# Kernel tuning notes

Hardware: AMD Instinct MI355X
Metric: run time of the kernel (lower is better)

Reference implementation:

```python
import jax, jax.numpy as jnp
import numpy as np

N_HEAD = 8


def build_mask(T, N):
    """Boolean mask [L, L], True = blocked. Mirrors the torch st_mask construction
    for text_mask_mode='part_only', text_to_motion_attn=False, all domains present."""
    L = 3 * T + 5 * N
    motion = 3 * T
    m = np.zeros((L, L), dtype=bool)
    # motion x motion: start fully blocked, then carve block-causal structure
    m[:motion, :motion] = True
    causal = np.tril(np.ones((T, T), dtype=bool))          # incl. diagonal
    strict = np.tril(np.ones((T, T), dtype=bool), k=-1)    # strictly lower
    m[0:T, 0:T] = ~causal
    m[T:2*T, 0:T] = ~causal
    m[T:2*T, T:2*T] = ~strict
    m[T:2*T, 2*T:3*T] = ~strict
    m[2*T:3*T, 0:T] = ~causal
    m[2*T:3*T, T:2*T] = ~causal
    m[2*T:3*T, 2*T:3*T] = ~strict
    # motion queries cannot see text keys
    m[:motion, motion:] = True
    # text queries cannot see motion keys (text_to_motion_attn=False)
    m[motion:, :motion] = True
    # part_only: upper-body rows see upper/torso/whole/simple_tag text domains;
    # lower-body rows see lower/torso/whole/simple_tag text domains
    ts = motion
    up, down = slice(T, 2*T), slice(2*T, 3*T)
    for d in (0, 2, 3, 4):
        m[up, ts + d*N: ts + (d+1)*N] = False
    for d in (1, 2, 3, 4):
        m[down, ts + d*N: ts + (d+1)*N] = False
    # text x text region stays all-False (full attention among text tokens)
    return jnp.asarray(m)


def setup_inputs() -> dict:
    key = jax.random.key(0)
    ks = jax.random.split(key, 9)
    B, T_motion, N, C = 2, 1024, 64, 512
    L = 3 * T_motion + 5 * N
    s = 1.0 / np.sqrt(C)
    return {
        "x": jax.random.normal(ks[0], (B, L, C), dtype=jnp.float32),
        "Wq": jax.random.normal(ks[1], (C, C), dtype=jnp.float32) * s,
        "bq": jnp.zeros((C,), dtype=jnp.float32),
        "Wk": jax.random.normal(ks[2], (C, C), dtype=jnp.float32) * s,
        "bk": jnp.zeros((C,), dtype=jnp.float32),
        "Wv": jax.random.normal(ks[3], (C, C), dtype=jnp.float32) * s,
        "bv": jnp.zeros((C,), dtype=jnp.float32),
        "Wp": jax.random.normal(ks[4], (C, C), dtype=jnp.float32) * s,
        "bp": jnp.zeros((C,), dtype=jnp.float32),
        "T_motion": T_motion,
        "N": N,
    }


def reference(x, Wq, bq, Wk, bk, Wv, bv, Wp, bp, T_motion, N):
    B, L, C = x.shape
    H = N_HEAD
    dh = C // H
    mask = build_mask(int(T_motion), int(N))  # [L, L] bool, True = blocked

    def split_heads(t):  # [B, L, C] -> [B, H, L, dh]
        return t.reshape(B, L, H, dh).transpose(0, 2, 1, 3)

    q = split_heads(x @ Wq + bq)
    k = split_heads(x @ Wk + bk)
    v = split_heads(x @ Wv + bv)

    att = jnp.einsum("bhqd,bhkd->bhqk", q, k) * (1.0 / np.sqrt(dh))
    att = jnp.where(mask[None, None], -jnp.inf, att)
    att = jax.nn.softmax(att, axis=-1)
    y = jnp.einsum("bhqk,bhkd->bhqd", att, v)
    y = y.transpose(0, 2, 1, 3).reshape(B, L, C)
    return y @ Wp + bp
```

## Files before the change

kernel.cpp:

```cpp
#include <hip/hip_runtime.h>
#include <hip/hip_bf16.h>
#include <math.h>

typedef __attribute__((ext_vector_type(8))) short bf16x8;
typedef __attribute__((ext_vector_type(4))) short short4v;
typedef __attribute__((ext_vector_type(4))) float f32x4;

#define DEVI __device__ __forceinline__

constexpr int Bb  = 2;
constexpr int Tm  = 1024;
constexpr int Ntx = 64;
constexpr int Hh  = 8;
constexpr int Ll  = 3*Tm + 5*Ntx;
constexpr int Mm  = Bb*Ll;
constexpr int MOT = 3*Tm;
constexpr int UPH = 75;
constexpr int PST = 72;

DEVI short f2b(float f) {
  unsigned u = __builtin_bit_cast(unsigned, f);
  u = u + 0x7fffu + ((u >> 16) & 1u);
  return (short)(u >> 16);
}

DEVI void gld16(const void* g, void* l) {
  __builtin_amdgcn_global_load_lds(
      (const __attribute__((address_space(1))) unsigned*)g,
      (__attribute__((address_space(3))) unsigned*)l, 16, 0, 0);
}

DEVI f32x4 mfma16(bf16x8 a, bf16x8 b, f32x4 c) {
  return __builtin_amdgcn_mfma_f32_16x16x32_bf16(a, b, c, 0, 0, 0);
}


__global__ __launch_bounds__(256) void cast_x_kern(const float* __restrict__ x,
                                                   short* __restrict__ xb) {
  int i = (blockIdx.x*256 + threadIdx.x)*4;
  float4 v = *(const float4*)(x + i);
  short4v r;
  r.x = f2b(v.x); r.y = f2b(v.y); r.z = f2b(v.z); r.w = f2b(v.w);
  *(short4v*)(xb + i) = r;
}

__global__ __launch_bounds__(256) void prep_w_kern(
    const float* __restrict__ Wq, const float* __restrict__ Wk,
    const float* __restrict__ Wv, const float* __restrict__ Wp,
    short* __restrict__ WtQKV, short* __restrict__ WpT) {
  int idx = blockIdx.x*256 + threadIdx.x;
  int mat = idx >> 18;
  int n = (idx >> 9) & 511;
  int k = idx & 511;
  const float* W = (mat == 0) ? Wq : (mat == 1) ? Wk : (mat == 2) ? Wv : Wp;
  short s = f2b(W[k*512 + n]);
  if (mat < 3) WtQKV[((size_t)(mat*512 + n))*512 + k] = s;
  else         WpT[(size_t)n*512 + k] = s;
}


template<int MODE>
__global__ __launch_bounds__(256) void gemm_bt(
    const short* __restrict__ A, const short* __restrict__ Bt,
    const float* __restrict__ bias_q, const float* __restrict__ bias_k,
    const float* __restrict__ bias_v,
    short* __restrict__ Qb, short* __restrict__ Kb, short* __restrict__ Vt,
    float* __restrict__ outf) {
  __shared__ __align__(16) short At[128*32];
  __shared__ __align__(16) short Bs[128*32];
  const int tid = threadIdx.x;
  const int w = tid >> 6, lane = tid & 63;
  const int col = lane & 15, g = lane >> 4;
  const int tm = blockIdx.x, tn = blockIdx.y;
  const int wm = w >> 1, wn = w & 1;

  f32x4 acc[4][4] = {};

  for (int k0 = 0; k0 < 512; k0 += 32) {
    __syncthreads();
#pragma unroll
    for (int it = 0; it < 2; ++it) {
      int e0 = w*512 + it*2048 + lane*8;
      int row = e0 >> 5, cc = e0 & 31;
      gld16(A  + (size_t)(tm*128 + row)*512 + k0 + cc, At + w*512 + it*2048);
      gld16(Bt + (size_t)(tn*128 + row)*512 + k0 + cc, Bs + w*512 + it*2048);
    }
    __syncthreads();
    bf16x8 af[4], bfr[4];
#pragma unroll
    for (int i = 0; i < 4; ++i)
      af[i] = *(const bf16x8*)(At + (wm*64 + i*16 + col)*32 + g*8);
#pragma unroll
    for (int j = 0; j < 4; ++j)
      bfr[j] = *(const bf16x8*)(Bs + (wn*64 + j*16 + col)*32 + g*8);
#pragma unroll
    for (int i = 0; i < 4; ++i)
#pragma unroll
      for (int j = 0; j < 4; ++j)
        acc[i][j] = mfma16(af[i], bfr[j], acc[i][j]);
  }

#pragma unroll
  for (int i = 0; i < 4; ++i) {
    int mbase = tm*128 + wm*64 + i*16 + g*4;
#pragma unroll
    for (int j = 0; j < 4; ++j) {
      int ncol = tn*128 + wn*64 + j*16 + col;
#pragma unroll
      for (int r = 0; r < 4; ++r) {
        int mrow = mbase + r;
        float v = acc[i][j][r];
        if constexpr (MODE == 0) {
          float bias = (ncol < 512) ? bias_q[ncol]
                     : (ncol < 1024) ? bias_k[ncol - 512] : bias_v[ncol - 1024];
          v += bias;
          int bb = (mrow >= Ll) ? 1 : 0;
          int lpos = mrow - bb*Ll;
          int nn = ncol & 511;
          int h = nn >> 6, dd = nn & 63;
          int bh = bb*8 + h;
          short s = f2b(v);
          if (ncol < 512)        Qb[((size_t)(bh*Ll + lpos))*64 + dd] = s;
          else if (ncol < 1024)  Kb[((size_t)(bh*Ll + lpos))*64 + dd] = s;
          else                   Vt[((size_t)(bh*64 + dd))*Ll + lpos] = s;
        } else {
          outf[(size_t)mrow*512 + ncol] = v + bias_q[ncol];
        }
      }
    }
  }
}


__global__ __launch_bounds__(256) void attn_kern(
    const short* __restrict__ Qb, const short* __restrict__ Kb,
    const short* __restrict__ Vt, float* __restrict__ slots,
    short* __restrict__ attout) {
  __shared__ __align__(16) short Kls[2][4096];
  __shared__ __align__(16) short Vls[2][4096];
  __shared__ __align__(16) short Pls[4][32*PST];
  const int tid = threadIdx.x;
  const int w = tid >> 6, lane = tid & 63;
  const int col = lane & 15, g = lane >> 4;

  const int v  = (blockIdx.x & 7)*150 + (blockIdx.x >> 3);
  const int bh = v / UPH;
  const int lr = v - bh*UPH;

  int qsec, seg = 0, j = 0, t3 = 0;
  if (lr < 56) {
    int jj = lr/7, s = lr - jj*7;
    j = 7 - jj;
    if (s == 0)      qsec = 0;
    else if (s <= 3) { qsec = 1; seg = s - 1; }
    else             { qsec = 2; seg = s - 4; }
  } else if (lr < 72) {
    int t = lr - 56; qsec = 1 + (t & 1); j = t >> 1; seg = 3;
  } else { qsec = 3; t3 = lr - 72; }

  const int q0b = (qsec < 3) ? qsec*Tm + j*128 : MOT + ((t3 == 2) ? 192 : t3*128);
  const int t0w = j*128 + w*32;
  const int q0w = q0b + w*32;

  int kbase = 0, off = 0, nb;
  bool masked;
  if (qsec == 3)      { kbase = MOT;  nb = 5;       masked = false; }
  else if (qsec == 0) { kbase = 0;    nb = 2*j + 2; masked = true; off = 0; }
  else if (seg == 0)  { kbase = 0;    nb = 2*j + 2; masked = true; off = 0; }
  else if (seg == 1)  { kbase = Tm;   nb = 2*j + 2; masked = true; off = (qsec == 1) ? 1 : 0; }
  else if (seg == 2)  { kbase = 2*Tm; nb = 2*j + 2; masked = true; off = 1; }
  else                { kbase = 0;    nb = 4;       masked = false; }

  auto keyof = [&](int i) -> int {
    if (qsec == 3) return MOT + i*64;
    if (!masked) { int d = (i == 0) ? ((qsec == 1) ? 0 : 1) : i + 1; return MOT + d*64; }
    return kbase + i*64;
  };

  const short* Kbase_ = Kb + (size_t)bh*Ll*64;
  const short* Vbase_ = Vt + (size_t)bh*64*Ll;

  bf16x8 aq[2][2];
#pragma unroll
  for (int qf = 0; qf < 2; ++qf) {
    const short* p = Qb + ((size_t)bh*Ll + q0w + qf*16 + col)*64;
    aq[qf][0] = *(const bf16x8*)(p + g*8);
    aq[qf][1] = *(const bf16x8*)(p + 32 + g*8);
  }

  float ls[2][4] = {};
  f32x4 out[2][4] = {};
  constexpr float SCl = 0.125f * 1.44269504f;

  auto stage = [&](int buf, int key0) {
#pragma unroll
    for (int it = 0; it < 2; ++it) {
      int L = it*4096 + tid*16;
      int row = L >> 7;
      int sw = (row & 7) << 4;
      gld16((const char*)Kbase_ + (size_t)key0*128 + (L ^ sw),
            (char*)&Kls[buf][0] + it*4096 + w*1024);
      gld16((const char*)(Vbase_ + (size_t)row*Ll + key0) + ((L & 127) ^ sw),
            (char*)&Vls[buf][0] + it*4096 + w*1024);
    }
  };

  auto compute = [&](int buf, int i) {
    const int swc = (col & 7) << 4;
    f32x4 s[2][4];
#pragma unroll
    for (int kk = 0; kk < 4; ++kk) {
      const char* base = (const char*)&Kls[buf][0] + (kk*16 + col)*128;
      bf16x8 k0 = *(const bf16x8*)(base + ((g*16) ^ swc));
      bf16x8 k1 = *(const bf16x8*)(base + ((64 + g*16) ^ swc));
#pragma unroll
      for (int qf = 0; qf < 2; ++qf) {
        f32x4 t = {0,0,0,0};
        t = mfma16(aq[qf][0], k0, t);
        t = mfma16(aq[qf][1], k1, t);
        s[qf][kk] = t;
      }
    }
    const bool dm = masked && (i*64 + 63 + off > t0w);
    short* pw = &Pls[w][0];
#pragma unroll
    for (int qf = 0; qf < 2; ++qf)
#pragma unroll
      for (int kk = 0; kk < 4; ++kk)
#pragma unroll
        for (int r = 0; r < 4; ++r) {
          float p = __builtin_amdgcn_exp2f(s[qf][kk][r]*SCl);
          if (dm && (i*64 + kk*16 + col + off > t0w + qf*16 + g*4 + r)) p = 0.f;
          ls[qf][r] += p;
          pw[(qf*16 + g*4 + r)*PST + kk*16 + col] = f2b(p);
        }
    bf16x8 pa[2][2];
#pragma unroll
    for (int qf = 0; qf < 2; ++qf) {
      const short* base = &Pls[w][0] + (qf*16 + col)*PST;
      pa[qf][0] = *(const bf16x8*)(base + g*8);
      pa[qf][1] = *(const bf16x8*)(base + 32 + g*8);
    }
#pragma unroll
    for (int ch = 0; ch < 4; ++ch) {
      const char* base = (const char*)&Vls[buf][0] + (ch*16 + col)*128;
      bf16x8 v0 = *(const bf16x8*)(base + ((g*16) ^ swc));
      bf16x8 v1 = *(const bf16x8*)(base + ((64 + g*16) ^ swc));
#pragma unroll
      for (int qf = 0; qf < 2; ++qf) {
        out[qf][ch] = mfma16(pa[qf][0], v0, out[qf][ch]);
        out[qf][ch] = mfma16(pa[qf][1], v1, out[qf][ch]);
      }
    }
  };

  stage(0, keyof(0));
  for (int i = 0; i < nb; ++i) {
    if (i + 1 < nb) {
      stage((i + 1) & 1, keyof(i + 1));
      asm volatile("s_waitcnt vmcnt(4)" ::: "memory");
    } else {
      asm volatile("s_waitcnt vmcnt(0)" ::: "memory");
    }
    __builtin_amdgcn_sched_barrier(0);
    __builtin_amdgcn_s_barrier();
    bool skip = masked && (t0w + 31 < i*64 + off);
    if (!skip) compute(i & 1, i);
    __builtin_amdgcn_s_barrier();
  }

  float rs[2][4];
#pragma unroll
  for (int qf = 0; qf < 2; ++qf)
#pragma unroll
    for (int r = 0; r < 4; ++r) {
      float t = ls[qf][r];
      t += __shfl_xor(t, 1); t += __shfl_xor(t, 2);
      t += __shfl_xor(t, 4); t += __shfl_xor(t, 8);
      rs[qf][r] = t;
    }

  if (qsec == 1 || qsec == 2) {
    float* sp = slots + ((((size_t)bh*2 + (qsec - 1))*8 + j)*4 + seg)*8320;
#pragma unroll
    for (int qf = 0; qf < 2; ++qf) {
#pragma unroll
      for (int ch = 0; ch < 4; ++ch)
#pragma unroll
        for (int r = 0; r < 4; ++r)
          sp[(w*32 + qf*16 + g*4 + r)*64 + ch*16 + col] = out[qf][ch][r];
      if (col == 0)
#pragma unroll
        for (int r = 0; r < 4; ++r)
          sp[8192 + w*32 + qf*16 + g*4 + r] = rs[qf][r];
    }
  } else {
    const int b = bh >> 3, h = bh & 7;
#pragma unroll
    for (int qf = 0; qf < 2; ++qf)
#pragma unroll
      for (int r = 0; r < 4; ++r) {
        float inv = 1.0f / rs[qf][r];
        size_t rowoff = ((size_t)(b*Ll + q0w + qf*16 + g*4 + r))*512 + h*64;
#pragma unroll
        for (int ch = 0; ch < 4; ++ch)
          attout[rowoff + ch*16 + col] = f2b(out[qf][ch][r]*inv);
      }
  }
}

__global__ __launch_bounds__(256) void fin_kern(const float* __restrict__ slots,
                                                short* __restrict__ attout) {
  const int w = threadIdx.x >> 6, lane = threadIdx.x & 63;
  const int ridx = blockIdx.x*4 + w;
  const int bh = ridx >> 11;
  const int rr = ridx & 2047;
  const int qsec = 1 + (rr >> 10);
  const int rl = rr & 1023;
  const int j = rl >> 7;
  const int row_local = rl & 127;
  const float* base = slots + (((size_t)bh*2 + (qsec - 1))*8 + j)*4*8320;
  float a = 0.f, l = 0.f;
#pragma unroll
  for (int s = 0; s < 4; ++s) {
    a += base[s*8320 + row_local*64 + lane];
    l += base[s*8320 + 8192 + row_local];
  }
  const int b = bh >> 3, h = bh & 7;
  attout[((size_t)(b*Ll + qsec*Tm + rl))*512 + h*64 + lane] = f2b(a / l);
}


extern "C" void kernel_launch(void* const* d_in, const int* in_sizes, int n_in,
                              void* d_out, int out_size, void* d_ws, size_t ws_size,
                              hipStream_t stream) {
  const float* x  = (const float*)d_in[0];
  const float* Wq = (const float*)d_in[1];
  const float* bq = (const float*)d_in[2];
  const float* Wk = (const float*)d_in[3];
  const float* bk = (const float*)d_in[4];
  const float* Wv = (const float*)d_in[5];
  const float* bv = (const float*)d_in[6];
  const float* Wp = (const float*)d_in[7];
  const float* bp = (const float*)d_in[8];
  float* out = (float*)d_out;

  short* ws = (short*)d_ws;
  constexpr size_t SZ  = (size_t)Mm*512;
  short* xb    = ws;
  short* WtQKV = xb + SZ;
  short* WpT   = WtQKV + (size_t)1536*512;
  short* Qb    = WpT + (size_t)512*512;
  short* Kb    = Qb + SZ;
  short* Vt    = Kb + SZ;
  short* att   = Vt + SZ;
  float* slots = (float*)(att + SZ);

  cast_x_kern<<<dim3(Mm*512/1024), dim3(256), 0, stream>>>(x, xb);
  prep_w_kern<<<dim3(4096), dim3(256), 0, stream>>>(Wq, Wk, Wv, Wp, WtQKV, WpT);
  gemm_bt<0><<<dim3(53, 12), dim3(256), 0, stream>>>(xb, WtQKV, bq, bk, bv,
                                                     Qb, Kb, Vt, nullptr);
  attn_kern<<<dim3(1200), dim3(256), 0, stream>>>(Qb, Kb, Vt, slots, att);
  fin_kern<<<dim3(8192), dim3(256), 0, stream>>>(slots, att);
  gemm_bt<1><<<dim3(53, 4), dim3(256), 0, stream>>>(att, WpT, bp, nullptr, nullptr,
                                                    nullptr, nullptr, nullptr, out);
}
```

Before: 109.5 us.

## Fold softmax scale into Q and transpose score MFMA for packed P stores

The scale 0.125*log2(e) is folded into Q when the projection epilogue writes it, which removes a multiply per score in the attention loop. The QK^T MFMA operands are swapped so each lane holds four consecutive keys for a single query. That lets P be converted with packed bf16 instructions and written to LDS as 8-byte stores instead of scalar shorts. Row sums now reduce with two shuffles instead of four per row, with a broadcast shuffle added in the direct-output path. The main risk is rounding from scaling Q before bf16 conversion.

Result: faster. 101.5 us (-7.4%).

```diff
diff --git a/kernel.cpp b/kernel.cpp
--- a/kernel.cpp
+++ b/kernel.cpp
@@ -5,6 +5,7 @@
 typedef __attribute__((ext_vector_type(8))) short bf16x8;
 typedef __attribute__((ext_vector_type(4))) short short4v;
 typedef __attribute__((ext_vector_type(4))) float f32x4;
+typedef __attribute__((ext_vector_type(2))) unsigned int u32x2;
 
 #define DEVI __device__ __forceinline__
 
@@ -119,10 +120,13 @@
           int nn = ncol & 511;
           int h = nn >> 6, dd = nn & 63;
           int bh = bb*8 + h;
-          short s = f2b(v);
-          if (ncol < 512)        Qb[((size_t)(bh*Ll + lpos))*64 + dd] = s;
-          else if (ncol < 1024)  Kb[((size_t)(bh*Ll + lpos))*64 + dd] = s;
-          else                   Vt[((size_t)(bh*64 + dd))*Ll + lpos] = s;
+          if (ncol < 512) {
+            Qb[((size_t)(bh*Ll + lpos))*64 + dd] = f2b(v*0.18033688f);
+          } else if (ncol < 1024) {
+            Kb[((size_t)(bh*Ll + lpos))*64 + dd] = f2b(v);
+          } else {
+            Vt[((size_t)(bh*64 + dd))*Ll + lpos] = f2b(v);
+          }
         } else {
           outf[(size_t)mrow*512 + ncol] = v + bias_q[ncol];
         }
@@ -187,10 +191,10 @@
     aq[qf][0] = *(const bf16x8*)(p + g*8);
     aq[qf][1] = *(const bf16x8*)(p + 32 + g*8);
   }
-
-  float ls[2][4] = {};
+  const int qv[2] = { t0w + col, t0w + 16 + col };
+
+  float ls[2] = {0.f, 0.f};
   f32x4 out[2][4] = {};
-  constexpr float SCl = 0.125f * 1.44269504f;
 
   auto stage = [&](int buf, int key0) {
 #pragma unroll
@@ -216,30 +220,40 @@
 #pragma unroll
       for (int qf = 0; qf < 2; ++qf) {
         f32x4 t = {0,0,0,0};
-        t = mfma16(aq[qf][0], k0, t);
-        t = mfma16(aq[qf][1], k1, t);
+        t = mfma16(k0, aq[qf][0], t);
+        t = mfma16(k1, aq[qf][1], t);
         s[qf][kk] = t;
       }
     }
     const bool dm = masked && (i*64 + 63 + off > t0w);
+    const int kl = i*64 + off + g*4;
     short* pw = &Pls[w][0];
 #pragma unroll
-    for (int qf = 0; qf < 2; ++qf)
-#pragma unroll
-      for (int kk = 0; kk < 4; ++kk)
+    for (int qf = 0; qf < 2; ++qf) {
+      float lsl = 0.f;
+#pragma unroll
+      for (int kk = 0; kk < 4; ++kk) {
+        float pe[4];
 #pragma unroll
         for (int r = 0; r < 4; ++r) {
-          float p = __builtin_amdgcn_exp2f(s[qf][kk][r]*SCl);
-          if (dm && (i*64 + kk*16 + col + off > t0w + qf*16 + g*4 + r)) p = 0.f;
-          ls[qf][r] += p;
-          pw[(qf*16 + g*4 + r)*PST + kk*16 + col] = f2b(p);
+          float p = __builtin_amdgcn_exp2f(s[qf][kk][r]);
+          if (dm && (kl + kk*16 + r > qv[qf])) p = 0.f;
+          pe[r] = p; lsl += p;
         }
+        unsigned pk0, pk1;
+        asm("v_cvt_pk_bf16_f32 %0, %1, %2" : "=v"(pk0) : "v"(pe[0]), "v"(pe[1]));
+        asm("v_cvt_pk_bf16_f32 %0, %1, %2" : "=v"(pk1) : "v"(pe[2]), "v"(pe[3]));
+        u32x2 pk; pk.x = pk0; pk.y = pk1;
+        *(u32x2*)(pw + (qf*16 + col)*PST + kk*16 + g*4) = pk;
+      }
+      ls[qf] += lsl;
+    }
     bf16x8 pa[2][2];
 #pragma unroll
     for (int qf = 0; qf < 2; ++qf) {
-      const short* base = &Pls[w][0] + (qf*16 + col)*PST;
-      pa[qf][0] = *(const bf16x8*)(base + g*8);
-      pa[qf][1] = *(const bf16x8*)(base + 32 + g*8);
+      const short* base2 = &Pls[w][0] + (qf*16 + col)*PST;
+      pa[qf][0] = *(const bf16x8*)(base2 + g*8);
+      pa[qf][1] = *(const bf16x8*)(base2 + 32 + g*8);
     }
 #pragma unroll
     for (int ch = 0; ch < 4; ++ch) {
@@ -269,16 +283,14 @@
     __builtin_amdgcn_s_barrier();
   }
 
-  float rs[2][4];
-#pragma unroll
-  for (int qf = 0; qf < 2; ++qf)
-#pragma unroll
-    for (int r = 0; r < 4; ++r) {
-      float t = ls[qf][r];
-      t += __shfl_xor(t, 1); t += __shfl_xor(t, 2);
-      t += __shfl_xor(t, 4); t += __shfl_xor(t, 8);
-      rs[qf][r] = t;
-    }
+  float rs[2];
+#pragma unroll
+  for (int qf = 0; qf < 2; ++qf) {
+    float t = ls[qf];
+    t += __shfl_xor(t, 16);
+    t += __shfl_xor(t, 32);
+    rs[qf] = t;
+  }
 
   if (qsec == 1 || qsec == 2) {
     float* sp = slots + ((((size_t)bh*2 + (qsec - 1))*8 + j)*4 + seg)*8320;
@@ -289,10 +301,8 @@
 #pragma unroll
         for (int r = 0; r < 4; ++r)
           sp[(w*32 + qf*16 + g*4 + r)*64 + ch*16 + col] = out[qf][ch][r];
-      if (col == 0)
-#pragma unroll
-        for (int r = 0; r < 4; ++r)
-          sp[8192 + w*32 + qf*16 + g*4 + r] = rs[qf][r];
+      if (g == 0)
+        sp[8192 + w*32 + qf*16 + col] = rs[qf];
     }
   } else {
     const int b = bh >> 3, h = bh & 7;
@@ -300,7 +310,8 @@
     for (int qf = 0; qf < 2; ++qf)
 #pragma unroll
       for (int r = 0; r < 4; ++r) {
-        float inv = 1.0f / rs[qf][r];
+        float dv = __shfl(rs[qf], g*4 + r);
+        float inv = 1.0f / dv;
         size_t rowoff = ((size_t)(b*Ll + q0w + qf*16 + g*4 + r))*512 + h*64;
 #pragma unroll
         for (int ch = 0; ch < 4; ++ch)
```
